# Kernel optimization log

Hardware: AMD Instinct MI355X
Metric: run time of the kernel (lower is better)

Reference implementation:

```python
import jax, jax.numpy as jnp
import numpy as np
import math

E = 256          # embed_dims
H = 8            # num_heads
ITER = 2         # iterative steps
PC_RANGE = (-140.8, -40.0, -3.0, 140.8, 40.0, 1.0)


def sine_embed(pos, num_feats):
    # pos: (..., 3) in (0,1); returns (..., 3*num_feats), per-coord interleaved sin/cos
    scale = 2.0 * math.pi
    i = jnp.arange(num_feats, dtype=jnp.float32)
    dim_t = 10000.0 ** (2.0 * jnp.floor(i / 2.0) / num_feats)
    p = pos[..., None] * scale / dim_t                      # (..., 3, F)
    emb = jnp.stack([jnp.sin(p[..., 0::2]), jnp.cos(p[..., 1::2])], axis=-1)
    emb = emb.reshape(p.shape[:-1] + (num_feats,))          # (..., 3, F)
    return emb.reshape(pos.shape[:-1] + (3 * num_feats,))


def mha(q, k, v, Wi, bi, Wo, bo, n_heads):
    # torch nn.MultiheadAttention math, seq-first layout: q (L,N,C), k/v (M,N,C)
    L, N, C = q.shape
    D = C // n_heads
    qp = (q @ Wi[:C].T + bi[:C]).reshape(L, N, n_heads, D)
    kp = (k @ Wi[C:2 * C].T + bi[C:2 * C]).reshape(k.shape[0], N, n_heads, D)
    vp = (v @ Wi[2 * C:].T + bi[2 * C:]).reshape(v.shape[0], N, n_heads, D)
    scores = jnp.einsum('lnhd,mnhd->nhlm', qp, kp) / math.sqrt(D)
    attn = jax.nn.softmax(scores, axis=-1)
    o = jnp.einsum('nhlm,mnhd->lnhd', attn, vp).reshape(L, N, C)
    return o @ Wo.T + bo


def setup_inputs() -> dict:
    key = jax.random.key(0)
    ks = jax.random.split(key, 12)
    Q, TOT, B, LMAX = 2048, 40, 8, 5
    s = 0.02
    return {
        'x': jax.random.normal(ks[0], (Q, TOT, E), jnp.float32),
        'reference_points': jax.random.uniform(ks[1], (TOT, Q, 3), jnp.float32),
        'pairwise_t_matrix': jax.random.normal(ks[2], (B, LMAX, LMAX, 4, 4), jnp.float32),
        'record_len': np.full((B,), 5, dtype=np.int64),
        'in_proj_w': jax.random.normal(ks[3], (3 * E, E), jnp.float32) * s,
        'in_proj_b': jnp.zeros((3 * E,), jnp.float32),
        'out_w': jax.random.normal(ks[4], (E, E), jnp.float32) * s,
        'out_b': jnp.zeros((E,), jnp.float32),
        'bev_w1': jax.random.normal(ks[5], (E, 3 * E), jnp.float32) * s,
        'bev_b1': jnp.zeros((E,), jnp.float32),
        'bev_w2': jax.random.normal(ks[6], (E, E), jnp.float32) * s,
        'bev_b2': jnp.zeros((E,), jnp.float32),
    }


def reference(x, reference_points, pairwise_t_matrix, in_proj_w, in_proj_b,
              out_w, out_b, bev_w1, bev_b1, bev_w2, bev_b2, record_len):
    rl = np.asarray(record_len)
    offsets = np.concatenate([[0], np.cumsum(rl)]).astype(int)
    lo = jnp.asarray(PC_RANGE[:3], jnp.float32)
    hi = jnp.asarray(PC_RANGE[3:], jnp.float32)

    x_cav = jnp.transpose(x, (1, 0, 2))                    # (total_cav, Q, C)
    ref = reference_points * (hi - lo) + lo                # un-normalize to pc_range

    outs = []
    for b in range(len(rl)):
        s, e = offsets[b], offsets[b + 1]
        n = e - s
        b_x = x_cav[s:e]                                   # (n, Q, C)
        if n == 1:
            outs.append(b_x)
            continue
        b_ref = ref[s:e]                                   # (n, Q, 3)
        t_ego = pairwise_t_matrix[b, :n, 0]                # (n, 4, 4) transform-to-ego
        homo = jnp.concatenate([b_ref, jnp.ones(b_ref.shape[:-1] + (1,), b_ref.dtype)], axis=-1)
        trans = jax.nn.sigmoid(jnp.einsum('nij,nqj->nqi', t_ego, homo)[..., :3])
        pe = sine_embed(trans, E)                          # (n, Q, 3E)
        bev = jax.nn.relu(pe @ bev_w1.T + bev_b1) @ bev_w2.T + bev_b2  # (n, Q, C)

        ego = b_x[0:1]
        neigh = b_x[1:]                                    # (n-1, Q, C)
        kk = neigh + bev[1:]
        for _ in range(ITER):
            q = jnp.broadcast_to(ego, neigh.shape)
            o = q + mha(q, kk, neigh, in_proj_w, in_proj_b, out_w, out_b, H)
            ego = jnp.sum(o, axis=0, keepdims=True)
        outs.append(jnp.concatenate([ego, neigh], axis=0))

    out = jnp.concatenate(outs, axis=0)                    # (total_cav, Q, C)
    return jnp.transpose(out, (1, 0, 2))                   # (Q, total_cav, C)
```

## Files before the change

kernel.cpp:

```cpp
#include <hip/hip_runtime.h>
#include <cstdint>
#include <cstddef>

typedef __bf16 bf16;
typedef __attribute__((ext_vector_type(8))) __bf16 bf16x8;
typedef __attribute__((ext_vector_type(4))) float f32x4;
typedef __attribute__((ext_vector_type(4))) unsigned int u32x4;

#define QN 2048

#if __has_builtin(__builtin_amdgcn_sinf)
#define SIN_REV(x) __builtin_amdgcn_sinf(x)
#define COS_REV(x) __builtin_amdgcn_cosf(x)
#else
#define SIN_REV(x) __sinf((x) * 6.283185307179586f)
#define COS_REV(x) __cosf((x) * 6.283185307179586f)
#endif

__device__ __forceinline__ float sigmoidf_(float v) { return 1.0f / (1.0f + __expf(-v)); }

__device__ __forceinline__ bf16x8 cvt8(const float* p) {
  const f32x4* p4 = (const f32x4*)p;
  f32x4 lo = p4[0], hi = p4[1];
  bf16x8 r;
#pragma unroll
  for (int j = 0; j < 4; ++j) { r[j] = (bf16)lo[j]; r[j + 4] = (bf16)hi[j]; }
  return r;
}

__device__ __forceinline__ void load_lds16(const bf16* g, bf16* l) {
  __builtin_amdgcn_global_load_lds(
      (const __attribute__((address_space(1))) void*)g,
      (__attribute__((address_space(3))) void*)l, 16, 0, 0);
}

__global__ __launch_bounds__(256) void setup_ker(
    const float* __restrict__ ipw, const float* __restrict__ ow,
    const float* __restrict__ w1, bf16* __restrict__ wb,
    const float* __restrict__ ipb, const float* __restrict__ w2f,
    const float* __restrict__ b2f, bf16* __restrict__ Wc,
    float* __restrict__ bkf) {
  __shared__ float row[256];
  __shared__ float red[256];
  if (blockIdx.x < 224) {
    int e = (blockIdx.x * 256 + threadIdx.x) * 8;
    const float* src; int off;
    if (e < 196608)      { src = ipw; off = e; }
    else if (e < 262144) { src = ow;  off = e - 196608; }
    else                 { src = w1;  off = e - 262144; }
    *(bf16x8*)(wb + e) = cvt8(src + off);
    return;
  }
  const int j = blockIdx.x - 224, l = threadIdx.x;
  row[l] = ipw[65536 + j * 256 + l];
  __syncthreads();
  float acc = 0.f;
#pragma unroll 4
  for (int m = 0; m < 256; ++m) acc += row[m] * w2f[m * 256 + l];
  Wc[(size_t)j * 512 + l] = (bf16)acc;
  Wc[(size_t)j * 512 + 256 + l] = (bf16)row[l];
  red[l] = row[l] * b2f[l];
  __syncthreads();
  for (int s = 128; s > 0; s >>= 1) {
    if (l < s) red[l] += red[l + s];
    __syncthreads();
  }
  if (l == 0) bkf[j] = ipb[256 + j] + red[0];
}

template <int AMODE, int EPI, int KDIM>
__device__ __forceinline__ void gemm_body(
    int bidx, bf16 (*As)[40], bf16 (*Bs)[32],
    const bf16* __restrict__ A, const bf16* __restrict__ W,
    const float* __restrict__ bias, const float* __restrict__ x,
    const float* __restrict__ rp, const float* __restrict__ pm,
    bf16* __restrict__ outB) {
  const int tid = threadIdx.x;
  const int bidm = bidx >> 1;
  const int bidn = bidx & 1;
  const int rowBase = bidm << 6;
  const int colBase = bidn << 7;

  const int wave = tid >> 6, lane = tid & 63;
  const int m16 = lane & 15, quad = lane >> 4;
  const int wr = wave >> 1, wc = wave & 1;

  const int sRow = tid >> 2, sq = tid & 3;
  const int rgA = rowBase + sRow;

  const float* afp = nullptr;
  float tr0 = 0.f, tr1 = 0.f, tr2 = 0.f;
  if constexpr (AMODE == 1) {
    int b = rgA >> 13, j = (rgA >> 11) & 3, q = rgA & 2047;
    int t = b * 5 + 1 + j;
    const float* rpp = rp + ((size_t)t * QN + q) * 3;
    float r0 = rpp[0] * 281.6f - 140.8f;
    float r1 = rpp[1] * 80.0f - 40.0f;
    float r2 = rpp[2] * 4.0f - 3.0f;
    const float* T = pm + (size_t)t * 80;
    tr0 = sigmoidf_(T[0] * r0 + T[1] * r1 + T[2] * r2 + T[3]);
    tr1 = sigmoidf_(T[4] * r0 + T[5] * r1 + T[6] * r2 + T[7]);
    tr2 = sigmoidf_(T[8] * r0 + T[9] * r1 + T[10] * r2 + T[11]);
  } else if constexpr (AMODE == 2 || AMODE == 5) {
    int b = rgA >> 13, j = (rgA >> 11) & 3, q = rgA & 2047;
    afp = x + (((size_t)q * 40 + b * 5 + 1 + j) << 8);
  }

  const bf16* wsrc = W + (size_t)(colBase + (wave << 5) + (lane >> 2)) * KDIM + ((lane & 3) << 3);
  bf16* bdst0 = &Bs[(wave << 5)][0];
  bf16* bdst1 = &Bs[(wave << 5) + 16][0];

  f32x4 acc[2][4] = {};

  for (int k0 = 0; k0 < KDIM; k0 += 32) {
    load_lds16(wsrc + k0, bdst0);
    load_lds16(wsrc + (size_t)16 * KDIM + k0, bdst1);

    bf16x8 a0;
    if constexpr (AMODE == 1) {
      int c = k0 >> 8;
      float tc = (c == 0) ? tr0 : (c == 1 ? tr1 : tr2);
      int ti0 = ((k0 & 255) + (sq << 3)) >> 1;
      float freq = exp2f((float)ti0 * -0.10381025296522975f);
#pragma unroll
      for (int p = 0; p < 4; ++p) {
        float ang = tc * freq;
        a0[2 * p]     = (bf16)SIN_REV(ang);
        a0[2 * p + 1] = (bf16)COS_REV(ang);
        freq *= 0.93057204092467f;
      }
    } else if constexpr (AMODE == 0) {
      a0 = *(const bf16x8*)(A + (size_t)rgA * KDIM + k0 + (sq << 3));
    } else if constexpr (AMODE == 5) {
      if (k0 < 256) {
        a0 = *(const bf16x8*)(A + ((size_t)rgA << 8) + k0 + (sq << 3));
      } else {
        a0 = cvt8(afp + (k0 - 256) + (sq << 3));
      }
    } else {
      a0 = cvt8(afp + k0 + (sq << 3));
    }
    *(bf16x8*)(&As[sRow][sq << 3]) = a0;
    __syncthreads();

    bf16x8 afr[2], bfr[4];
#pragma unroll
    for (int mt = 0; mt < 2; ++mt)
      afr[mt] = *(const bf16x8*)(&As[(wr << 5) + (mt << 4) + m16][quad << 3]);
#pragma unroll
    for (int nt = 0; nt < 4; ++nt)
      bfr[nt] = *(const bf16x8*)(&Bs[(wc << 6) + (nt << 4) + m16][quad << 3]);
#pragma unroll
    for (int mt = 0; mt < 2; ++mt)
#pragma unroll
      for (int nt = 0; nt < 4; ++nt)
        acc[mt][nt] = __builtin_amdgcn_mfma_f32_16x16x32_bf16(
            afr[mt], bfr[nt], acc[mt][nt], 0, 0, 0);
    __syncthreads();
  }

#pragma unroll
  for (int mt = 0; mt < 2; ++mt) {
#pragma unroll
    for (int nt = 0; nt < 4; ++nt) {
      const int col = colBase + (wc << 6) + (nt << 4) + m16;
      const float bv = bias[col];
#pragma unroll
      for (int rg = 0; rg < 4; ++rg) {
        const int r = rowBase + (wr << 5) + (mt << 4) + (quad << 2) + rg;
        float v = acc[mt][nt][rg] + bv;
        if constexpr (EPI == 0) {
          outB[(size_t)r * 256 + col] = (bf16)fmaxf(v, 0.0f);
        } else {
          outB[(size_t)r * 256 + col] = (bf16)v;
        }
      }
    }
  }
}

template <int AMODE, int EPI, int KDIM>
__global__ __launch_bounds__(256) void gemm_ker(
    const bf16* __restrict__ A, const bf16* __restrict__ W,
    const float* __restrict__ bias, const float* __restrict__ x,
    const float* __restrict__ rp, const float* __restrict__ pm,
    bf16* __restrict__ outB) {
  __shared__ bf16 As[64][40];
  __shared__ bf16 Bs[128][32];
  gemm_body<AMODE, EPI, KDIM>(blockIdx.x, As, Bs, A, W, bias, x, rp, pm, outB);
}

__global__ __launch_bounds__(256) void mega_ker(
    const bf16* __restrict__ w1b, const float* __restrict__ b1,
    const bf16* __restrict__ wv, const float* __restrict__ bv,
    const float* __restrict__ x, const float* __restrict__ rp,
    const float* __restrict__ pm, bf16* __restrict__ h,
    bf16* __restrict__ vp, float* __restrict__ out) {
  __shared__ bf16 As[64][40];
  __shared__ bf16 Bs[128][32];
  if (blockIdx.x < 2048) {
    gemm_body<1, 0, 768>(blockIdx.x, As, Bs, nullptr, w1b, b1, x, rp, pm, h);
  } else if (blockIdx.x < 4096) {
    gemm_body<2, 2, 256>(blockIdx.x - 2048, As, Bs, nullptr, wv, bv, x, rp, pm, vp);
  } else {
    int i = (blockIdx.x - 4096) * 256 + threadIdx.x;
    int t = (i >> 6) % 40;
    if ((t % 5) != 0) ((u32x4*)out)[i] = ((const u32x4*)x)[i];
  }
}

__device__ __forceinline__ void proj32db(const bf16 (*AP)[256],
                                         bf16 (*BsP)[256][32],
                                         const bf16* __restrict__ WB,
                                         f32x4 (*acc)[4], int wave, int lane) {
  const int m16 = lane & 15, quad = lane >> 4;
#define PSTAGE(P_, K_)                                                        \
  { _Pragma("unroll") for (int i_ = 0; i_ < 4; ++i_) {                        \
      const bf16* src_ = WB +                                                 \
          (size_t)((wave << 6) + (i_ << 4) + (lane >> 2)) * 256 + (K_) +      \
          ((lane & 3) << 3);                                                  \
      load_lds16(src_, &BsP[P_][(wave << 6) + (i_ << 4)][0]); } }
  PSTAGE(0, 0);
#pragma unroll
  for (int t = 0; t < 8; ++t) {
    const int p = t & 1;
    if (t < 7) {
      PSTAGE(p ^ 1, (t + 1) << 5);
      asm volatile("s_waitcnt vmcnt(4)" ::: "memory");
    } else {
      asm volatile("s_waitcnt vmcnt(0)" ::: "memory");
    }
    __builtin_amdgcn_sched_barrier(0);
    const int k0 = t << 5;
    bf16x8 afr[2], bfr[4];
#pragma unroll
    for (int mt = 0; mt < 2; ++mt) {
      const int r = (mt << 4) + m16;
      afr[mt] = *(const bf16x8*)(&AP[r][(((k0 >> 3) + quad) ^ (r & 7)) << 3]);
    }
#pragma unroll
    for (int nt = 0; nt < 4; ++nt)
      bfr[nt] = *(const bf16x8*)(&BsP[p][(wave << 6) + (nt << 4) + m16][quad << 3]);
#pragma unroll
    for (int mt = 0; mt < 2; ++mt)
#pragma unroll
      for (int nt = 0; nt < 4; ++nt)
        acc[mt][nt] = __builtin_amdgcn_mfma_f32_16x16x32_bf16(
            afr[mt], bfr[nt], acc[mt][nt], 0, 0, 0);
  }
#undef PSTAGE
}

__device__ __forceinline__ void attn_phase(bf16 (*P)[256],
                                           const bf16* __restrict__ kp,
                                           const bf16* __restrict__ vp,
                                           int rowBase, int tid) {
  const int r = tid >> 3, h = tid & 7;
  const int re = rowBase + r, b = re >> 11, q = re & 2047;
  float qv[32];
#pragma unroll
  for (int i = 0; i < 4; ++i) {
    bf16x8 t = *(const bf16x8*)(&P[r][((((h << 2) + i)) ^ (r & 7)) << 3]);
#pragma unroll
    for (int j = 0; j < 8; ++j) qv[i * 8 + j] = (float)t[j];
  }
  const size_t base = ((size_t)(b * 4) * QN + q) * 256 + h * 32;
  float s[4];
#pragma unroll
  for (int m = 0; m < 4; ++m) {
    const bf16x8* kv = (const bf16x8*)(kp + base + (size_t)m * (QN * 256));
    float a = 0.f;
#pragma unroll
    for (int i = 0; i < 4; ++i) {
      bf16x8 t = kv[i];
#pragma unroll
      for (int j = 0; j < 8; ++j) a += qv[i * 8 + j] * (float)t[j];
    }
    s[m] = a * 0.17677669529663687f;
  }
  float mx = fmaxf(fmaxf(s[0], s[1]), fmaxf(s[2], s[3]));
  float e0 = __expf(s[0] - mx), e1 = __expf(s[1] - mx);
  float e2 = __expf(s[2] - mx), e3 = __expf(s[3] - mx);
  float inv = 1.0f / (e0 + e1 + e2 + e3);
  float w[4] = {e0 * inv, e1 * inv, e2 * inv, e3 * inv};
  float ov[32] = {};
#pragma unroll
  for (int m = 0; m < 4; ++m) {
    const bf16x8* vv = (const bf16x8*)(vp + base + (size_t)m * (QN * 256));
#pragma unroll
    for (int i = 0; i < 4; ++i) {
      bf16x8 t = vv[i];
#pragma unroll
      for (int j = 0; j < 8; ++j) ov[i * 8 + j] += w[m] * (float)t[j];
    }
  }
#pragma unroll
  for (int i = 0; i < 4; ++i) {
    bf16x8 t;
#pragma unroll
    for (int j = 0; j < 8; ++j) t[j] = (bf16)ov[i * 8 + j];
    *(bf16x8*)(&P[r][((((h << 2) + i)) ^ (r & 7)) << 3]) = t;
  }
}

__global__ __launch_bounds__(256, 2) void iter_ker(
    const bf16* __restrict__ kp, const bf16* __restrict__ vp,
    const bf16* __restrict__ wq, const bf16* __restrict__ owb,
    const float* __restrict__ qb, const float* __restrict__ ob,
    const float* __restrict__ x, float* __restrict__ out) {
  __shared__ bf16 P1[32][256];
  __shared__ bf16 P2[32][256];
  __shared__ bf16 Bs[2][256][32];

  const int tid = threadIdx.x;
  const int rowBase = blockIdx.x << 5;
  const int wave = tid >> 6, lane = tid & 63;
  const int m16 = lane & 15, quad = lane >> 4;

  {
    const int r = tid >> 3, e = tid & 7;
    const int re = rowBase + r, b = re >> 11, q = re & 2047;
    const float* src = x + (((size_t)q * 40 + b * 5) << 8) + (e << 5);
#pragma unroll
    for (int s = 0; s < 4; ++s) {
      bf16x8 v = cvt8(src + s * 8);
      *(bf16x8*)(&P1[r][((((e << 2) + s)) ^ (r & 7)) << 3]) = v;
    }
  }
  __syncthreads();

  float e1r[2][4][4];
  f32x4 acc[2][4];

#define ZACC                                                                  \
  { _Pragma("unroll") for (int mt = 0; mt < 2; ++mt)                          \
    _Pragma("unroll") for (int nt = 0; nt < 4; ++nt) {                        \
      f32x4 z = {0.f, 0.f, 0.f, 0.f}; acc[mt][nt] = z; } }

#define QEPI                                                                  \
  { _Pragma("unroll") for (int mt = 0; mt < 2; ++mt)                          \
    _Pragma("unroll") for (int nt = 0; nt < 4; ++nt) {                        \
      const int col = (wave << 6) + (nt << 4) + m16;                          \
      const float bv = qb[col];                                               \
      _Pragma("unroll") for (int rg = 0; rg < 4; ++rg) {                      \
        const int row = (mt << 4) + (quad << 2) + rg;                         \
        P2[row][(((col >> 3) ^ (row & 7)) << 3) + (col & 7)] =                \
            (bf16)(acc[mt][nt][rg] + bv);                                     \
      } } }

  ZACC;
  proj32db(P1, Bs, wq, acc, wave, lane);
  QEPI;
  __syncthreads();
  attn_phase(P2, kp, vp, rowBase, tid);
  __syncthreads();
  ZACC;
  proj32db(P2, Bs, owb, acc, wave, lane);
#pragma unroll
  for (int mt = 0; mt < 2; ++mt)
#pragma unroll
    for (int nt = 0; nt < 4; ++nt) {
      const int col = (wave << 6) + (nt << 4) + m16;
      const float bv = ob[col];
#pragma unroll
      for (int rg = 0; rg < 4; ++rg) {
        const int row = (mt << 4) + (quad << 2) + rg;
        const int re = rowBase + row, b = re >> 11, q = re & 2047;
        float xe = x[(((size_t)q * 40 + b * 5) << 8) + col];
        float e1 = 4.0f * (xe + acc[mt][nt][rg] + bv);
        e1r[mt][nt][rg] = e1;
        P1[row][(((col >> 3) ^ (row & 7)) << 3) + (col & 7)] = (bf16)e1;
      }
    }
  __syncthreads();

  ZACC;
  proj32db(P1, Bs, wq, acc, wave, lane);
  QEPI;
  __syncthreads();
  attn_phase(P2, kp, vp, rowBase, tid);
  __syncthreads();
  ZACC;
  proj32db(P2, Bs, owb, acc, wave, lane);
#pragma unroll
  for (int mt = 0; mt < 2; ++mt)
#pragma unroll
    for (int nt = 0; nt < 4; ++nt) {
      const int col = (wave << 6) + (nt << 4) + m16;
      const float bv = ob[col];
#pragma unroll
      for (int rg = 0; rg < 4; ++rg) {
        const int row = (mt << 4) + (quad << 2) + rg;
        const int re = rowBase + row, b = re >> 11, q = re & 2047;
        out[(((size_t)q * 40 + b * 5) << 8) + col] =
            4.0f * (e1r[mt][nt][rg] + acc[mt][nt][rg] + bv);
      }
    }
#undef ZACC
#undef QEPI
}

extern "C" void kernel_launch(void* const* d_in, const int* in_sizes, int n_in,
                              void* d_out, int out_size, void* d_ws, size_t ws_size,
                              hipStream_t stream) {
  (void)n_in; (void)out_size; (void)ws_size;
  const float* x   = (const float*)d_in[0];
  const float* rp  = (const float*)d_in[1];
  const float* pm  = (const float*)d_in[2];
  const int wbase = (in_sizes[3] == 8) ? 4 : 3;
  const float* ipw = (const float*)d_in[wbase + 0];
  const float* ipb = (const float*)d_in[wbase + 1];
  const float* ow  = (const float*)d_in[wbase + 2];
  const float* obv = (const float*)d_in[wbase + 3];
  const float* w1  = (const float*)d_in[wbase + 4];
  const float* b1  = (const float*)d_in[wbase + 5];
  const float* w2  = (const float*)d_in[wbase + 6];
  const float* b2  = (const float*)d_in[wbase + 7];
  float* out = (float*)d_out;
  char* ws = (char*)d_ws;

  bf16* h    = (bf16*)(ws + 0);
  bf16* kp   = (bf16*)(ws + 33554432);
  bf16* vp   = (bf16*)(ws + 67108864);
  bf16* wb   = (bf16*)(ws + 100663296);
  bf16* Wc   = (bf16*)(ws + 101711872);
  float* bkf = (float*)(ws + 101974016);
  const bf16* wq  = wb;
  const bf16* wv  = wb + 131072;
  const bf16* owb = wb + 196608;
  const bf16* w1b = wb + 262144;

  setup_ker<<<480, 256, 0, stream>>>(ipw, ow, w1, wb, ipb, w2, b2, Wc, bkf);
  mega_ker<<<24576, 256, 0, stream>>>(w1b, b1, wv, ipb + 512, x, rp, pm, h, vp, out);
  gemm_ker<5, 2, 512><<<2048, 256, 0, stream>>>(h, Wc, bkf, x, rp, pm, kp);
  iter_ker<<<512, 256, 0, stream>>>(kp, vp, wq, owb, ipb, obv, x, out);
}
```

Measured before the change: 354.9 us.

## Fuse BEV MLP first and second GEMMs with full-width tiles in mega kernel

Merges the positional-encoding MLP GEMM and the key-projection GEMM into a single block that holds the ReLU hidden tile in LDS, so the intermediate h buffer no longer goes to global memory and one kernel launch disappears. Tiles become 64x256 per block with each wave covering 64 columns and 4x4 MFMA accumulators. The value projection uses the same layout, and the copy of the non-ego rows to the output becomes a grid-stride loop over 2048 blocks. The costs are more LDS per block (about 50KB) and more accumulator registers, which may reduce occupancy.

```diff
diff --git a/kernel.cpp b/kernel.cpp
--- a/kernel.cpp
+++ b/kernel.cpp
@@ -68,145 +68,187 @@
   if (l == 0) bkf[j] = ipb[256 + j] + red[0];
 }
 
-template <int AMODE, int EPI, int KDIM>
-__device__ __forceinline__ void gemm_body(
-    int bidx, bf16 (*As)[40], bf16 (*Bs)[32],
-    const bf16* __restrict__ A, const bf16* __restrict__ W,
-    const float* __restrict__ bias, const float* __restrict__ x,
-    const float* __restrict__ rp, const float* __restrict__ pm,
-    bf16* __restrict__ outB) {
+__global__ __launch_bounds__(256) void mega_ker(
+    const bf16* __restrict__ w1b, const float* __restrict__ b1,
+    const bf16* __restrict__ Wc, const float* __restrict__ bkf,
+    const bf16* __restrict__ wv, const float* __restrict__ bv,
+    const float* __restrict__ x, const float* __restrict__ rp,
+    const float* __restrict__ pm, bf16* __restrict__ kp,
+    bf16* __restrict__ vp, float* __restrict__ out) {
+  __shared__ bf16 As[64][40];
+  __shared__ bf16 Bs[256][32];
+  __shared__ bf16 hT[64][264];
+
   const int tid = threadIdx.x;
-  const int bidm = bidx >> 1;
-  const int bidn = bidx & 1;
-  const int rowBase = bidm << 6;
-  const int colBase = bidn << 7;
-
   const int wave = tid >> 6, lane = tid & 63;
   const int m16 = lane & 15, quad = lane >> 4;
-  const int wr = wave >> 1, wc = wave & 1;
-
   const int sRow = tid >> 2, sq = tid & 3;
+
+  if (blockIdx.x >= 2048) {
+    for (int i = (blockIdx.x - 2048) * 256 + tid; i < 5242880; i += 524288) {
+      int t = (i >> 6) % 40;
+      if ((t % 5) != 0) ((u32x4*)out)[i] = ((const u32x4*)x)[i];
+    }
+    return;
+  }
+
+  const bool isPE = blockIdx.x < 1024;
+  const int rowBase = (isPE ? blockIdx.x : blockIdx.x - 1024) << 6;
   const int rgA = rowBase + sRow;
-
-  const float* afp = nullptr;
-  float tr0 = 0.f, tr1 = 0.f, tr2 = 0.f;
-  if constexpr (AMODE == 1) {
-    int b = rgA >> 13, j = (rgA >> 11) & 3, q = rgA & 2047;
-    int t = b * 5 + 1 + j;
+  const int b = rgA >> 13, j = (rgA >> 11) & 3, q = rgA & 2047;
+  const float* afp = x + (((size_t)q * 40 + b * 5 + 1 + j) << 8);
+
+  f32x4 acc[4][4] = {};
+
+  if (isPE) {
+    const int t = b * 5 + 1 + j;
     const float* rpp = rp + ((size_t)t * QN + q) * 3;
     float r0 = rpp[0] * 281.6f - 140.8f;
     float r1 = rpp[1] * 80.0f - 40.0f;
     float r2 = rpp[2] * 4.0f - 3.0f;
     const float* T = pm + (size_t)t * 80;
-    tr0 = sigmoidf_(T[0] * r0 + T[1] * r1 + T[2] * r2 + T[3]);
-    tr1 = sigmoidf_(T[4] * r0 + T[5] * r1 + T[6] * r2 + T[7]);
-    tr2 = sigmoidf_(T[8] * r0 + T[9] * r1 + T[10] * r2 + T[11]);
-  } else if constexpr (AMODE == 2 || AMODE == 5) {
-    int b = rgA >> 13, j = (rgA >> 11) & 3, q = rgA & 2047;
-    afp = x + (((size_t)q * 40 + b * 5 + 1 + j) << 8);
-  }
-
-  const bf16* wsrc = W + (size_t)(colBase + (wave << 5) + (lane >> 2)) * KDIM + ((lane & 3) << 3);
-  bf16* bdst0 = &Bs[(wave << 5)][0];
-  bf16* bdst1 = &Bs[(wave << 5) + 16][0];
-
-  f32x4 acc[2][4] = {};
-
-  for (int k0 = 0; k0 < KDIM; k0 += 32) {
-    load_lds16(wsrc + k0, bdst0);
-    load_lds16(wsrc + (size_t)16 * KDIM + k0, bdst1);
-
-    bf16x8 a0;
-    if constexpr (AMODE == 1) {
-      int c = k0 >> 8;
-      float tc = (c == 0) ? tr0 : (c == 1 ? tr1 : tr2);
-      int ti0 = ((k0 & 255) + (sq << 3)) >> 1;
-      float freq = exp2f((float)ti0 * -0.10381025296522975f);
-#pragma unroll
-      for (int p = 0; p < 4; ++p) {
-        float ang = tc * freq;
-        a0[2 * p]     = (bf16)SIN_REV(ang);
-        a0[2 * p + 1] = (bf16)COS_REV(ang);
-        freq *= 0.93057204092467f;
-      }
-    } else if constexpr (AMODE == 0) {
-      a0 = *(const bf16x8*)(A + (size_t)rgA * KDIM + k0 + (sq << 3));
-    } else if constexpr (AMODE == 5) {
+    const float tr0 = sigmoidf_(T[0] * r0 + T[1] * r1 + T[2] * r2 + T[3]);
+    const float tr1 = sigmoidf_(T[4] * r0 + T[5] * r1 + T[6] * r2 + T[7]);
+    const float tr2 = sigmoidf_(T[8] * r0 + T[9] * r1 + T[10] * r2 + T[11]);
+
+    const bf16* ws1 = w1b + (size_t)((wave << 6) + (lane >> 2)) * 768 + ((lane & 3) << 3);
+    for (int k0 = 0; k0 < 768; k0 += 32) {
+#pragma unroll
+      for (int i = 0; i < 4; ++i)
+        load_lds16(ws1 + (size_t)(i << 4) * 768 + k0, &Bs[(wave << 6) + (i << 4)][0]);
+      bf16x8 a0;
+      {
+        int c = k0 >> 8;
+        float tc = (c == 0) ? tr0 : (c == 1 ? tr1 : tr2);
+        int ti0 = ((k0 & 255) + (sq << 3)) >> 1;
+        float freq = exp2f((float)ti0 * -0.10381025296522975f);
+#pragma unroll
+        for (int p = 0; p < 4; ++p) {
+          float ang = tc * freq;
+          a0[2 * p]     = (bf16)SIN_REV(ang);
+          a0[2 * p + 1] = (bf16)COS_REV(ang);
+          freq *= 0.93057204092467f;
+        }
+      }
+      *(bf16x8*)(&As[sRow][sq << 3]) = a0;
+      __syncthreads();
+      bf16x8 afr[4], bfr[4];
+#pragma unroll
+      for (int mt = 0; mt < 4; ++mt)
+        afr[mt] = *(const bf16x8*)(&As[(mt << 4) + m16][quad << 3]);
+#pragma unroll
+      for (int nt = 0; nt < 4; ++nt)
+        bfr[nt] = *(const bf16x8*)(&Bs[(wave << 6) + (nt << 4) + m16][quad << 3]);
+#pragma unroll
+      for (int mt = 0; mt < 4; ++mt)
+#pragma unroll
+        for (int nt = 0; nt < 4; ++nt)
+          acc[mt][nt] = __builtin_amdgcn_mfma_f32_16x16x32_bf16(
+              afr[mt], bfr[nt], acc[mt][nt], 0, 0, 0);
+      __syncthreads();
+    }
+#pragma unroll
+    for (int mt = 0; mt < 4; ++mt)
+#pragma unroll
+      for (int nt = 0; nt < 4; ++nt) {
+        const int col = (wave << 6) + (nt << 4) + m16;
+        const float bvv = b1[col];
+#pragma unroll
+        for (int rg = 0; rg < 4; ++rg) {
+          const int row = (mt << 4) + (quad << 2) + rg;
+          hT[row][col] = (bf16)fmaxf(acc[mt][nt][rg] + bvv, 0.0f);
+        }
+      }
+    __syncthreads();
+
+#pragma unroll
+    for (int mt = 0; mt < 4; ++mt)
+#pragma unroll
+      for (int nt = 0; nt < 4; ++nt) {
+        f32x4 z = {0.f, 0.f, 0.f, 0.f};
+        acc[mt][nt] = z;
+      }
+    const bf16* ws2 = Wc + (size_t)((wave << 6) + (lane >> 2)) * 512 + ((lane & 3) << 3);
+    for (int k0 = 0; k0 < 512; k0 += 32) {
+#pragma unroll
+      for (int i = 0; i < 4; ++i)
+        load_lds16(ws2 + (size_t)(i << 4) * 512 + k0, &Bs[(wave << 6) + (i << 4)][0]);
+      if (k0 >= 256) {
+        bf16x8 a0 = cvt8(afp + (k0 - 256) + (sq << 3));
+        *(bf16x8*)(&As[sRow][sq << 3]) = a0;
+      }
+      __syncthreads();
+      bf16x8 afr[4], bfr[4];
       if (k0 < 256) {
-        a0 = *(const bf16x8*)(A + ((size_t)rgA << 8) + k0 + (sq << 3));
+#pragma unroll
+        for (int mt = 0; mt < 4; ++mt)
+          afr[mt] = *(const bf16x8*)(&hT[(mt << 4) + m16][k0 + (quad << 3)]);
       } else {
-        a0 = cvt8(afp + (k0 - 256) + (sq << 3));
-      }
-    } else {
-      a0 = cvt8(afp + k0 + (sq << 3));
-    }
+#pragma unroll
+        for (int mt = 0; mt < 4; ++mt)
+          afr[mt] = *(const bf16x8*)(&As[(mt << 4) + m16][quad << 3]);
+      }
+#pragma unroll
+      for (int nt = 0; nt < 4; ++nt)
+        bfr[nt] = *(const bf16x8*)(&Bs[(wave << 6) + (nt << 4) + m16][quad << 3]);
+#pragma unroll
+      for (int mt = 0; mt < 4; ++mt)
+#pragma unroll
+        for (int nt = 0; nt < 4; ++nt)
+          acc[mt][nt] = __builtin_amdgcn_mfma_f32_16x16x32_bf16(
+              afr[mt], bfr[nt], acc[mt][nt], 0, 0, 0);
+      __syncthreads();
+    }
+#pragma unroll
+    for (int mt = 0; mt < 4; ++mt)
+#pragma unroll
+      for (int nt = 0; nt < 4; ++nt) {
+        const int col = (wave << 6) + (nt << 4) + m16;
+        const float bvv = bkf[col];
+#pragma unroll
+        for (int rg = 0; rg < 4; ++rg) {
+          const int r = rowBase + (mt << 4) + (quad << 2) + rg;
+          kp[(size_t)r * 256 + col] = (bf16)(acc[mt][nt][rg] + bvv);
+        }
+      }
+    return;
+  }
+
+  const bf16* wsV = wv + (size_t)((wave << 6) + (lane >> 2)) * 256 + ((lane & 3) << 3);
+  for (int k0 = 0; k0 < 256; k0 += 32) {
+#pragma unroll
+    for (int i = 0; i < 4; ++i)
+      load_lds16(wsV + (size_t)(i << 4) * 256 + k0, &Bs[(wave << 6) + (i << 4)][0]);
+    bf16x8 a0 = cvt8(afp + k0 + (sq << 3));
     *(bf16x8*)(&As[sRow][sq << 3]) = a0;
     __syncthreads();
-
-    bf16x8 afr[2], bfr[4];
-#pragma unroll
-    for (int mt = 0; mt < 2; ++mt)
-      afr[mt] = *(const bf16x8*)(&As[(wr << 5) + (mt << 4) + m16][quad << 3]);
+    bf16x8 afr[4], bfr[4];
+#pragma unroll
+    for (int mt = 0; mt < 4; ++mt)
+      afr[mt] = *(const bf16x8*)(&As[(mt << 4) + m16][quad << 3]);
 #pragma unroll
     for (int nt = 0; nt < 4; ++nt)
-      bfr[nt] = *(const bf16x8*)(&Bs[(wc << 6) + (nt << 4) + m16][quad << 3]);
-#pragma unroll
-    for (int mt = 0; mt < 2; ++mt)
+      bfr[nt] = *(const bf16x8*)(&Bs[(wave << 6) + (nt << 4) + m16][quad << 3]);
+#pragma unroll
+    for (int mt = 0; mt < 4; ++mt)
 #pragma unroll
       for (int nt = 0; nt < 4; ++nt)
         acc[mt][nt] = __builtin_amdgcn_mfma_f32_16x16x32_bf16(
             afr[mt], bfr[nt], acc[mt][nt], 0, 0, 0);
     __syncthreads();
   }
-
-#pragma unroll
-  for (int mt = 0; mt < 2; ++mt) {
+#pragma unroll
+  for (int mt = 0; mt < 4; ++mt)
 #pragma unroll
     for (int nt = 0; nt < 4; ++nt) {
-      const int col = colBase + (wc << 6) + (nt << 4) + m16;
-      const float bv = bias[col];
+      const int col = (wave << 6) + (nt << 4) + m16;
+      const float bvv = bv[col];
 #pragma unroll
       for (int rg = 0; rg < 4; ++rg) {
-        const int r = rowBase + (wr << 5) + (mt << 4) + (quad << 2) + rg;
-        float v = acc[mt][nt][rg] + bv;
-        if constexpr (EPI == 0) {
-          outB[(size_t)r * 256 + col] = (bf16)fmaxf(v, 0.0f);
-        } else {
-          outB[(size_t)r * 256 + col] = (bf16)v;
-        }
-      }
-    }
-  }
-}
-
-template <int AMODE, int EPI, int KDIM>
-__global__ __launch_bounds__(256) void gemm_ker(
-    const bf16* __restrict__ A, const bf16* __restrict__ W,
-    const float* __restrict__ bias, const float* __restrict__ x,
-    const float* __restrict__ rp, const float* __restrict__ pm,
-    bf16* __restrict__ outB) {
-  __shared__ bf16 As[64][40];
-  __shared__ bf16 Bs[128][32];
-  gemm_body<AMODE, EPI, KDIM>(blockIdx.x, As, Bs, A, W, bias, x, rp, pm, outB);
-}
-
-__global__ __launch_bounds__(256) void mega_ker(
-    const bf16* __restrict__ w1b, const float* __restrict__ b1,
-    const bf16* __restrict__ wv, const float* __restrict__ bv,
-    const float* __restrict__ x, const float* __restrict__ rp,
-    const float* __restrict__ pm, bf16* __restrict__ h,
-    bf16* __restrict__ vp, float* __restrict__ out) {
-  __shared__ bf16 As[64][40];
-  __shared__ bf16 Bs[128][32];
-  if (blockIdx.x < 2048) {
-    gemm_body<1, 0, 768>(blockIdx.x, As, Bs, nullptr, w1b, b1, x, rp, pm, h);
-  } else if (blockIdx.x < 4096) {
-    gemm_body<2, 2, 256>(blockIdx.x - 2048, As, Bs, nullptr, wv, bv, x, rp, pm, vp);
-  } else {
-    int i = (blockIdx.x - 4096) * 256 + threadIdx.x;
-    int t = (i >> 6) % 40;
-    if ((t % 5) != 0) ((u32x4*)out)[i] = ((const u32x4*)x)[i];
-  }
+        const int r = rowBase + (mt << 4) + (quad << 2) + rg;
+        vp[(size_t)r * 256 + col] = (bf16)(acc[mt][nt][rg] + bvv);
+      }
+    }
 }
 
 __device__ __forceinline__ void proj32db(const bf16 (*AP)[256],
@@ -419,7 +461,6 @@
   float* out = (float*)d_out;
   char* ws = (char*)d_ws;
 
-  bf16* h    = (bf16*)(ws + 0);
   bf16* kp   = (bf16*)(ws + 33554432);
   bf16* vp   = (bf16*)(ws + 67108864);
   bf16* wb   = (bf16*)(ws + 100663296);
@@ -431,7 +472,7 @@
   const bf16* w1b = wb + 262144;
 
   setup_ker<<<480, 256, 0, stream>>>(ipw, ow, w1, wb, ipb, w2, b2, Wc, bkf);
-  mega_ker<<<24576, 256, 0, stream>>>(w1b, b1, wv, ipb + 512, x, rp, pm, h, vp, out);
-  gemm_ker<5, 2, 512><<<2048, 256, 0, stream>>>(h, Wc, bkf, x, rp, pm, kp);
+  mega_ker<<<4096, 256, 0, stream>>>(w1b, b1, Wc, bkf, wv, ipb + 512,
+                                     x, rp, pm, kp, vp, out);
   iter_ker<<<512, 256, 0, stream>>>(kp, vp, wq, owb, ipb, obv, x, out);
 }
```

Result: faster. 340.4 us (-4.1%).
